# Performance work log

Measured on AMD Instinct MI355X. Metric: run time of the kernel, lower is better.

Reference implementation:

```python
import jax, jax.numpy as jnp
import numpy as np

# Per-layer (in_dim, hidden) for the 6 stacked LSTM layers:
# rnn_inp: (1,64),(64,64),(64,64); rnn_out: (64,1),(1,1),(1,1)
_LAYER_DIMS = [(1, 64), (64, 64), (64, 64), (64, 1), (1, 1), (1, 1)]
_LAYER_NAMES = ['a0', 'a1', 'a2', 'b0', 'b1', 'b2']


def _lstm_layer(x, w_ih, w_hh, b_ih, b_hh):
    """Single unidirectional LSTM layer, PyTorch gate order (i, f, g, o).
    x: [B, T, Din]; w_ih: [4H, Din]; w_hh: [4H, H]; biases: [4H]. Returns [B, T, H]."""
    H = w_hh.shape[1]
    B = x.shape[0]
    # Input projection for all timesteps at once (one big GEMM).
    pre = jnp.einsum('btd,gd->btg', x, w_ih) + b_ih + b_hh  # [B, T, 4H]
    pre_t = jnp.swapaxes(pre, 0, 1)  # [T, B, 4H]

    def step(carry, xt):
        h, c = carry
        gates = xt + h @ w_hh.T  # [B, 4H]
        i, f, g, o = jnp.split(gates, 4, axis=-1)
        i = jax.nn.sigmoid(i)
        f = jax.nn.sigmoid(f)
        g = jnp.tanh(g)
        o = jax.nn.sigmoid(o)
        c = f * c + i * g
        h = o * jnp.tanh(c)
        return (h, c), h

    h0 = jnp.zeros((B, H), x.dtype)
    (_, _), hs = jax.lax.scan(step, (h0, h0), pre_t)  # hs: [T, B, H]
    return jnp.swapaxes(hs, 0, 1)


def setup_inputs() -> dict:
    key = jax.random.key(0)
    B, T = 256, 512
    inp = {}
    k, key = jax.random.split(key)
    inp['x'] = jax.random.normal(k, (B, T, 1), dtype=jnp.float32)
    for name, (din, h) in zip(_LAYER_NAMES, _LAYER_DIMS):
        s = 1.0 / np.sqrt(h)  # PyTorch LSTM init scale U(-1/sqrt(H), 1/sqrt(H))
        k1, k2, k3, k4, key = jax.random.split(key, 5)
        inp[f'w_ih_{name}'] = jax.random.uniform(k1, (4 * h, din), jnp.float32, -s, s)
        inp[f'w_hh_{name}'] = jax.random.uniform(k2, (4 * h, h), jnp.float32, -s, s)
        inp[f'b_ih_{name}'] = jax.random.uniform(k3, (4 * h,), jnp.float32, -s, s)
        inp[f'b_hh_{name}'] = jax.random.uniform(k4, (4 * h,), jnp.float32, -s, s)
    return inp


def reference(x,
              w_ih_a0, w_hh_a0, b_ih_a0, b_hh_a0,
              w_ih_a1, w_hh_a1, b_ih_a1, b_hh_a1,
              w_ih_a2, w_hh_a2, b_ih_a2, b_hh_a2,
              w_ih_b0, w_hh_b0, b_ih_b0, b_hh_b0,
              w_ih_b1, w_hh_b1, b_ih_b1, b_hh_b1,
              w_ih_b2, w_hh_b2, b_ih_b2, b_hh_b2):
    layers = [
        (w_ih_a0, w_hh_a0, b_ih_a0, b_hh_a0),
        (w_ih_a1, w_hh_a1, b_ih_a1, b_hh_a1),
        (w_ih_a2, w_hh_a2, b_ih_a2, b_hh_a2),
        (w_ih_b0, w_hh_b0, b_ih_b0, b_hh_b0),
        (w_ih_b1, w_hh_b1, b_ih_b1, b_hh_b1),
        (w_ih_b2, w_hh_b2, b_ih_b2, b_hh_b2),
    ]
    h = x
    for w_ih, w_hh, b_ih, b_hh in layers:
        h = _lstm_layer(h, w_ih, w_hh, b_ih, b_hh)
    # activation between the two LSTM stacks is identity (activation_type='identity')
    return h  # [B, T, 1]
```

## Files before the change

### kernel.cpp

```cpp
#include <hip/hip_runtime.h>


#define BB 256
#define TT 512
#define CH 8
#define NS 16
#define NW (TT / CH)
#define HP 72
#define PP 260

typedef _Float16 v2h __attribute__((ext_vector_type(2)));
typedef _Float16 v8h __attribute__((ext_vector_type(8)));
typedef float v4f __attribute__((ext_vector_type(4)));

__device__ __forceinline__ float sig_(float x) {
  return __builtin_amdgcn_rcpf(1.f + __builtin_amdgcn_exp2f(-1.44269504f * x));
}
__device__ __forceinline__ float tanh_(float x) {
  return __builtin_fmaf(2.f, __builtin_amdgcn_rcpf(1.f + __builtin_amdgcn_exp2f(-2.88539008f * x)), -1.f);
}

template <int K>
__device__ __forceinline__ float qb_(float v) {
  return __int_as_float(__builtin_amdgcn_update_dpp(
      0, __float_as_int(v), (K | (K << 2) | (K << 4) | (K << 6)), 0xF, 0xF, true));
}

#if __has_builtin(__builtin_amdgcn_fdot2)
#define FDOT2(acc, a, b) (acc) = __builtin_amdgcn_fdot2((a), (b), (acc), false)
#else
#define FDOT2(acc, a, b) \
  (acc) = __builtin_fmaf((float)(a)[0], (float)(b)[0], \
          __builtin_fmaf((float)(a)[1], (float)(b)[1], (acc)))
#endif
#define KEEPP(a) asm volatile("" : "+v"(a))
#define PIN32(w)                                                            \
  do {                                                                      \
    _Pragma("unroll") for (int _i = 0; _i < 32; ++_i) KEEPP((w)[_i]);       \
  } while (0)
#define PIN16(w)                                                            \
  do {                                                                      \
    _Pragma("unroll") for (int _i = 0; _i < 16; ++_i) KEEPP((w)[_i]);       \
  } while (0)

#define WAITP(i, v)                                                           \
  while (__hip_atomic_load(&prog[i], __ATOMIC_ACQUIRE,                        \
                           __HIP_MEMORY_SCOPE_WORKGROUP) < (v)) {             \
    __builtin_amdgcn_s_sleep(1);                                              \
  }
#define POSTP(i, v)                                                           \
  do {                                                                        \
    asm volatile("s_waitcnt lgkmcnt(0)" ::: "memory");                        \
    if (lane == 0)                                                            \
      __hip_atomic_store(&prog[i], (v), __ATOMIC_RELEASE,                     \
                         __HIP_MEMORY_SCOPE_WORKGROUP);                       \
  } while (0)

__device__ __forceinline__ v2h bc2h_(int v) { return __builtin_bit_cast(v2h, v); }

__device__ __forceinline__ void load_h64(const _Float16* p, v2h hv[32]) {
  const int4* hp = reinterpret_cast<const int4*>(p);
#pragma unroll
  for (int i = 0; i < 8; ++i) {
    int4 blk = hp[i];
    hv[4 * i + 0] = bc2h_(blk.x);
    hv[4 * i + 1] = bc2h_(blk.y);
    hv[4 * i + 2] = bc2h_(blk.z);
    hv[4 * i + 3] = bc2h_(blk.w);
  }
}

__device__ __forceinline__ void load_row16(const float* src, v2h dst[32]) {
  const float4* p = reinterpret_cast<const float4*>(src);
#pragma unroll
  for (int i = 0; i < 16; ++i) {
    float4 v = p[i];
    dst[2 * i]     = v2h{(_Float16)v.x, (_Float16)v.y};
    dst[2 * i + 1] = v2h{(_Float16)v.z, (_Float16)v.w};
  }
}

__device__ __forceinline__ void load_row_pair(const float* src, v2h* lo, v2h* hi) {
  const float4* p = reinterpret_cast<const float4*>(src);
#pragma unroll
  for (int i = 0; i < 8; ++i) {
    float4 v = p[i];
    lo[2 * i]     = v2h{(_Float16)v.x, (_Float16)v.y};
    lo[2 * i + 1] = v2h{(_Float16)v.z, (_Float16)v.w};
  }
#pragma unroll
  for (int i = 0; i < 8; ++i) {
    float4 v = p[8 + i];
    hi[2 * i]     = v2h{(_Float16)v.x, (_Float16)v.y};
    hi[2 * i + 1] = v2h{(_Float16)v.z, (_Float16)v.w};
  }
}

__device__ __forceinline__ v8h ldbfrag_(const float* W, int t, int kc, int lane) {
  const int row = 16 * t + (lane & 15);
  const float* p = W + row * 64 + 32 * kc + 4 * (lane >> 4);
  float4 fa = *reinterpret_cast<const float4*>(p);
  float4 fb = *reinterpret_cast<const float4*>(p + 16);
  return v8h{(_Float16)fa.x, (_Float16)fa.y, (_Float16)fa.z, (_Float16)fa.w,
             (_Float16)fb.x, (_Float16)fb.y, (_Float16)fb.z, (_Float16)fb.w};
}

__device__ __forceinline__ void dot4_(const v2h w[4][32], const v2h hv[32],
                                      float& p0, float& p1, float& p2, float& p3) {
  float a0 = p0, a1 = p1, a2 = p2, a3 = p3;
  float b0 = 0.f, b1 = 0.f, b2 = 0.f, b3 = 0.f;
#pragma unroll
  for (int j = 0; j < 32; j += 2) {
    FDOT2(a0, w[0][j], hv[j]);         FDOT2(a1, w[1][j], hv[j]);
    FDOT2(a2, w[2][j], hv[j]);         FDOT2(a3, w[3][j], hv[j]);
    FDOT2(b0, w[0][j + 1], hv[j + 1]); FDOT2(b1, w[1][j + 1], hv[j + 1]);
    FDOT2(b2, w[2][j + 1], hv[j + 1]); FDOT2(b3, w[3][j + 1], hv[j + 1]);
  }
  p0 = a0 + b0; p1 = a1 + b1; p2 = a2 + b2; p3 = a3 + b3;
}

__global__ __attribute__((amdgpu_flat_work_group_size(384, 384),
                          amdgpu_waves_per_eu(2, 2)))
void lstm_pipe_k(
    const float* __restrict__ x,
    const float* __restrict__ wih_a0, const float* __restrict__ whh_a0,
    const float* __restrict__ bih_a0, const float* __restrict__ bhh_a0,
    const float* __restrict__ wih_a1, const float* __restrict__ whh_a1,
    const float* __restrict__ bih_a1, const float* __restrict__ bhh_a1,
    const float* __restrict__ wih_a2, const float* __restrict__ whh_a2,
    const float* __restrict__ bih_a2, const float* __restrict__ bhh_a2,
    const float* __restrict__ wih_b0, const float* __restrict__ whh_b0,
    const float* __restrict__ bih_b0, const float* __restrict__ bhh_b0,
    const float* __restrict__ wih_b1, const float* __restrict__ whh_b1,
    const float* __restrict__ bih_b1, const float* __restrict__ bhh_b1,
    const float* __restrict__ wih_b2, const float* __restrict__ whh_b2,
    const float* __restrict__ bih_b2, const float* __restrict__ bhh_b2,
    float* __restrict__ out)
{
  const int b = blockIdx.x;
  const int tid = threadIdx.x;
  const int wave = tid >> 6;
  const int lane = tid & 63;

  __shared__ __align__(16) _Float16 hh[3][NS][HP];
  __shared__ __align__(16) float pj[2][NS][PP];
  __shared__ float xs[TT];
  __shared__ int prog[6];

  for (int i = tid; i < TT; i += 384) xs[i] = x[(size_t)b * TT + i];
  for (int i = tid; i < 3 * NS * HP / 2; i += 384) reinterpret_cast<int*>(hh)[i] = 0;
  if (tid < 6) prog[tid] = 0;

  union UW {
    v2h wt[4][32];
    v8h bfr[16][2];
  } u;

  float bias[4] = {0.f, 0.f, 0.f, 0.f};
  float wi0_[4] = {0.f, 0.f, 0.f, 0.f};
  float whb0[4] = {}, wi1b[4] = {}, wh1b[4] = {}, bb1[4] = {},
        wi2b[4] = {}, wh2b[4] = {}, bb2[4] = {};

  if (wave == 0) {
#pragma unroll
    for (int q = 0; q < 4; ++q) {
      const int row = q * 64 + lane;
      load_row16(whh_a0 + row * 64, u.wt[q]);
      bias[q] = bih_a0[row] + bhh_a0[row];
      wi0_[q] = wih_a0[row];
    }
    PIN32(u.wt[0]); PIN32(u.wt[1]); PIN32(u.wt[2]); PIN32(u.wt[3]);
  } else if (wave == 1) {
#pragma unroll
    for (int q = 0; q < 4; ++q) {
      const int row = q * 64 + lane;
      load_row16(whh_a1 + row * 64, u.wt[q]);
      bias[q] = bih_a1[row] + bhh_a1[row];
    }
    PIN32(u.wt[0]); PIN32(u.wt[1]); PIN32(u.wt[2]); PIN32(u.wt[3]);
  } else if (wave == 2) {
#pragma unroll
    for (int q = 0; q < 4; ++q) {
      const int row = q * 64 + lane;
      load_row16(whh_a2 + row * 64, u.wt[q]);
      bias[q] = bih_a2[row] + bhh_a2[row];
    }
    PIN32(u.wt[0]); PIN32(u.wt[1]); PIN32(u.wt[2]); PIN32(u.wt[3]);
  } else if (wave == 3) {
    const int q = lane & 3;
    load_row_pair(wih_b0 + q * 64, u.wt[0], u.wt[1]);
    bias[0] = bih_b0[q] + bhh_b0[q];
#pragma unroll
    for (int k = 0; k < 4; ++k) {
      whb0[k] = whh_b0[k];
      wi1b[k] = wih_b1[k]; wh1b[k] = whh_b1[k]; bb1[k] = bih_b1[k] + bhh_b1[k];
      wi2b[k] = wih_b2[k]; wh2b[k] = whh_b2[k]; bb2[k] = bih_b2[k] + bhh_b2[k];
    }
    PIN16(u.wt[0]); PIN16(u.wt[1]);
  } else if (wave == 4) {
#pragma unroll
    for (int t = 0; t < 16; ++t) {
      u.bfr[t][0] = ldbfrag_(wih_a1, t, 0, lane);
      u.bfr[t][1] = ldbfrag_(wih_a1, t, 1, lane);
    }
  } else {
#pragma unroll
    for (int t = 0; t < 16; ++t) {
      u.bfr[t][0] = ldbfrag_(wih_a2, t, 0, lane);
      u.bfr[t][1] = ldbfrag_(wih_a2, t, 1, lane);
    }
  }
  __syncthreads();

  float c = 0.f;
  float h0b = 0.f, c0b = 0.f, h1b = 0.f, c1b = 0.f, h2b = 0.f, c2b = 0.f;

  if (wave == 0) {
    __builtin_amdgcn_s_setprio(1);
    for (int k = 0; k < NW; ++k) {
      if (k >= 2) { WAITP(4, k - 1); }
      const int t0 = k * CH;
      for (int s = 0; s < CH; ++s) {
        const int t = t0 + s;
        v2h hv[32];
        load_h64(&hh[0][(t + NS - 1) & (NS - 1)][0], hv);
        const float xv = xs[t];
        float p0 = bias[0], p1 = bias[1], p2 = bias[2], p3 = bias[3];
        dot4_(u.wt, hv, p0, p1, p2, p3);
        p0 = __builtin_fmaf(wi0_[0], xv, p0);
        p1 = __builtin_fmaf(wi0_[1], xv, p1);
        p2 = __builtin_fmaf(wi0_[2], xv, p2);
        p3 = __builtin_fmaf(wi0_[3], xv, p3);
        float gi = sig_(p0), gf = sig_(p1), gg = tanh_(p2), go = sig_(p3);
        c = __builtin_fmaf(gf, c, gi * gg);
        hh[0][t & (NS - 1)][lane] = (_Float16)(go * tanh_(c));
      }
      POSTP(0, k + 1);
    }
    __builtin_amdgcn_s_setprio(0);
  } else if (wave == 1) {
    __builtin_amdgcn_s_setprio(1);
    for (int k = 0; k < NW; ++k) {
      WAITP(4, k + 1);
      if (k >= 2) { WAITP(5, k - 1); }
      const int t0 = k * CH;
      for (int s = 0; s < CH; ++s) {
        const int t = t0 + s;
        v2h hv[32];
        load_h64(&hh[1][(t + NS - 1) & (NS - 1)][0], hv);
        float4 pr = *reinterpret_cast<const float4*>(&pj[0][t & (NS - 1)][lane * 4]);
        float p0 = bias[0], p1 = bias[1], p2 = bias[2], p3 = bias[3];
        dot4_(u.wt, hv, p0, p1, p2, p3);
        p0 += pr.x; p1 += pr.y; p2 += pr.z; p3 += pr.w;
        float gi = sig_(p0), gf = sig_(p1), gg = tanh_(p2), go = sig_(p3);
        c = __builtin_fmaf(gf, c, gi * gg);
        hh[1][t & (NS - 1)][lane] = (_Float16)(go * tanh_(c));
      }
      POSTP(1, k + 1);
    }
    __builtin_amdgcn_s_setprio(0);
  } else if (wave == 2) {
    __builtin_amdgcn_s_setprio(1);
    for (int k = 0; k < NW; ++k) {
      WAITP(5, k + 1);
      if (k >= 2) { WAITP(3, k - 1); }
      const int t0 = k * CH;
      for (int s = 0; s < CH; ++s) {
        const int t = t0 + s;
        v2h hv[32];
        load_h64(&hh[2][(t + NS - 1) & (NS - 1)][0], hv);
        float4 pr = *reinterpret_cast<const float4*>(&pj[1][t & (NS - 1)][lane * 4]);
        float p0 = bias[0], p1 = bias[1], p2 = bias[2], p3 = bias[3];
        dot4_(u.wt, hv, p0, p1, p2, p3);
        p0 += pr.x; p1 += pr.y; p2 += pr.z; p3 += pr.w;
        float gi = sig_(p0), gf = sig_(p1), gg = tanh_(p2), go = sig_(p3);
        c = __builtin_fmaf(gf, c, gi * gg);
        hh[2][t & (NS - 1)][lane] = (_Float16)(go * tanh_(c));
      }
      POSTP(2, k + 1);
    }
    __builtin_amdgcn_s_setprio(0);
  } else if (wave == 3) {
    for (int k = 0; k < NW; ++k) {
      WAITP(2, k + 1);
      const int t0 = k * CH;
      for (int s = 0; s < CH; ++s) {
        const int t = t0 + s;
        v2h hv[32];
        load_h64(&hh[2][t & (NS - 1)][0], hv);
        float pga = bias[0], pgb = 0.f;
#pragma unroll
        for (int j = 0; j < 16; ++j) {
          FDOT2(pga, u.wt[0][j], hv[j]);
          FDOT2(pgb, u.wt[1][j], hv[16 + j]);
        }
        float pg = pga + pgb;
        float p_i = qb_<0>(pg), p_f = qb_<1>(pg), p_g = qb_<2>(pg), p_o = qb_<3>(pg);
        float i0 = sig_(__builtin_fmaf(whb0[0], h0b, p_i));
        float f0 = sig_(__builtin_fmaf(whb0[1], h0b, p_f));
        float g0 = tanh_(__builtin_fmaf(whb0[2], h0b, p_g));
        float o0 = sig_(__builtin_fmaf(whb0[3], h0b, p_o));
        c0b = __builtin_fmaf(f0, c0b, i0 * g0);
        h0b = o0 * tanh_(c0b);
        float i1 = sig_(bb1[0] + __builtin_fmaf(wi1b[0], h0b, wh1b[0] * h1b));
        float f1 = sig_(bb1[1] + __builtin_fmaf(wi1b[1], h0b, wh1b[1] * h1b));
        float g1 = tanh_(bb1[2] + __builtin_fmaf(wi1b[2], h0b, wh1b[2] * h1b));
        float o1 = sig_(bb1[3] + __builtin_fmaf(wi1b[3], h0b, wh1b[3] * h1b));
        c1b = __builtin_fmaf(f1, c1b, i1 * g1);
        h1b = o1 * tanh_(c1b);
        float i2 = sig_(bb2[0] + __builtin_fmaf(wi2b[0], h1b, wh2b[0] * h2b));
        float f2 = sig_(bb2[1] + __builtin_fmaf(wi2b[1], h1b, wh2b[1] * h2b));
        float g2 = tanh_(bb2[2] + __builtin_fmaf(wi2b[2], h1b, wh2b[2] * h2b));
        float o2 = sig_(bb2[3] + __builtin_fmaf(wi2b[3], h1b, wh2b[3] * h2b));
        c2b = __builtin_fmaf(f2, c2b, i2 * g2);
        h2b = o2 * tanh_(c2b);
        if (lane == 0) out[(size_t)b * TT + t] = h2b;
      }
      POSTP(3, k + 1);
    }
  } else if (wave == 4) {
    for (int k = 0; k < NW; ++k) {
      WAITP(0, k + 1);
      if (k >= 2) { WAITP(1, k - 1); }
      const int t0 = k * CH;
      const int slotb = (t0 + (lane & 15)) & (NS - 1);
      const char* hp = (const char*)(&hh[0][slotb][0]) + 8 * (lane >> 4);
      int2 r00 = *(const int2*)(hp);
      int2 r01 = *(const int2*)(hp + 32);
      int2 r10 = *(const int2*)(hp + 64);
      int2 r11 = *(const int2*)(hp + 96);
      v8h Bf0 = __builtin_bit_cast(v8h, int4{r00.x, r00.y, r01.x, r01.y});
      v8h Bf1 = __builtin_bit_cast(v8h, int4{r10.x, r10.y, r11.x, r11.y});
      float* pbase = &pj[0][slotb][0] + 16 * (lane >> 4);
      const bool wr = (lane & 15) < 8;
      const v4f z = {0.f, 0.f, 0.f, 0.f};
#pragma unroll
      for (int tl = 0; tl < 16; ++tl) {
        v4f acc = __builtin_amdgcn_mfma_f32_16x16x32_f16(u.bfr[tl][0], Bf0, z, 0, 0, 0);
        acc = __builtin_amdgcn_mfma_f32_16x16x32_f16(u.bfr[tl][1], Bf1, acc, 0, 0, 0);
        if (wr) {
          const int o = 64 * (tl & 3) + (tl >> 2);
          pbase[o] = acc[0]; pbase[o + 4] = acc[1];
          pbase[o + 8] = acc[2]; pbase[o + 12] = acc[3];
        }
        __builtin_amdgcn_sched_barrier(0);
      }
      POSTP(4, k + 1);
    }
  } else {
    for (int k = 0; k < NW; ++k) {
      WAITP(1, k + 1);
      if (k >= 2) { WAITP(2, k - 1); }
      const int t0 = k * CH;
      const int slotb = (t0 + (lane & 15)) & (NS - 1);
      const char* hp = (const char*)(&hh[1][slotb][0]) + 8 * (lane >> 4);
      int2 r00 = *(const int2*)(hp);
      int2 r01 = *(const int2*)(hp + 32);
      int2 r10 = *(const int2*)(hp + 64);
      int2 r11 = *(const int2*)(hp + 96);
      v8h Bf0 = __builtin_bit_cast(v8h, int4{r00.x, r00.y, r01.x, r01.y});
      v8h Bf1 = __builtin_bit_cast(v8h, int4{r10.x, r10.y, r11.x, r11.y});
      float* pbase = &pj[1][slotb][0] + 16 * (lane >> 4);
      const bool wr = (lane & 15) < 8;
      const v4f z = {0.f, 0.f, 0.f, 0.f};
#pragma unroll
      for (int tl = 0; tl < 16; ++tl) {
        v4f acc = __builtin_amdgcn_mfma_f32_16x16x32_f16(u.bfr[tl][0], Bf0, z, 0, 0, 0);
        acc = __builtin_amdgcn_mfma_f32_16x16x32_f16(u.bfr[tl][1], Bf1, acc, 0, 0, 0);
        if (wr) {
          const int o = 64 * (tl & 3) + (tl >> 2);
          pbase[o] = acc[0]; pbase[o + 4] = acc[1];
          pbase[o + 8] = acc[2]; pbase[o + 12] = acc[3];
        }
        __builtin_amdgcn_sched_barrier(0);
      }
      POSTP(5, k + 1);
    }
  }
}

extern "C" void kernel_launch(void* const* d_in, const int* in_sizes, int n_in,
                              void* d_out, int out_size, void* d_ws, size_t ws_size,
                              hipStream_t stream) {
  const float* x      = (const float*)d_in[0];
  const float* wih_a0 = (const float*)d_in[1];
  const float* whh_a0 = (const float*)d_in[2];
  const float* bih_a0 = (const float*)d_in[3];
  const float* bhh_a0 = (const float*)d_in[4];
  const float* wih_a1 = (const float*)d_in[5];
  const float* whh_a1 = (const float*)d_in[6];
  const float* bih_a1 = (const float*)d_in[7];
  const float* bhh_a1 = (const float*)d_in[8];
  const float* wih_a2 = (const float*)d_in[9];
  const float* whh_a2 = (const float*)d_in[10];
  const float* bih_a2 = (const float*)d_in[11];
  const float* bhh_a2 = (const float*)d_in[12];
  const float* wih_b0 = (const float*)d_in[13];
  const float* whh_b0 = (const float*)d_in[14];
  const float* bih_b0 = (const float*)d_in[15];
  const float* bhh_b0 = (const float*)d_in[16];
  const float* wih_b1 = (const float*)d_in[17];
  const float* whh_b1 = (const float*)d_in[18];
  const float* bih_b1 = (const float*)d_in[19];
  const float* bhh_b1 = (const float*)d_in[20];
  const float* wih_b2 = (const float*)d_in[21];
  const float* whh_b2 = (const float*)d_in[22];
  const float* bih_b2 = (const float*)d_in[23];
  const float* bhh_b2 = (const float*)d_in[24];
  float* out = (float*)d_out;

  lstm_pipe_k<<<BB, 384, 0, stream>>>(
      x,
      wih_a0, whh_a0, bih_a0, bhh_a0,
      wih_a1, whh_a1, bih_a1, bhh_a1,
      wih_a2, whh_a2, bih_a2, bhh_a2,
      wih_b0, whh_b0, bih_b0, bhh_b0,
      wih_b1, whh_b1, bih_b1, bhh_b1,
      wih_b2, whh_b2, bih_b2, bhh_b2,
      out);
}
```

Before: 347.5 us.

## Use MFMA for recurrent h@W_hh in 64-wide LSTM waves and shrink chunk size

Replaces the per-lane fdot2 dot products for the recurrent matrix-vector product in the three 64-hidden layers with MFMA 16x16x32 f16 ops. The weight fragments are loaded in MFMA B layout and the needed output column is picked out per lane with selects. The pipeline chunk size drops from 8 to 4 timesteps and the dependency waits are adjusted, which shortens pipeline fill latency between stages. This wastes most of each MFMA, since only one row of the 16-row A tile is used, and it adds selection overhead per step.

Result: faster. 338.4 us (-2.6%).

```diff
diff --git a/kernel.cpp b/kernel.cpp
--- a/kernel.cpp
+++ b/kernel.cpp
@@ -3,7 +3,7 @@
 
 #define BB 256
 #define TT 512
-#define CH 8
+#define CH 4
 #define NS 16
 #define NW (TT / CH)
 #define HP 72
@@ -34,10 +34,6 @@
           __builtin_fmaf((float)(a)[1], (float)(b)[1], (acc)))
 #endif
 #define KEEPP(a) asm volatile("" : "+v"(a))
-#define PIN32(w)                                                            \
-  do {                                                                      \
-    _Pragma("unroll") for (int _i = 0; _i < 32; ++_i) KEEPP((w)[_i]);       \
-  } while (0)
 #define PIN16(w)                                                            \
   do {                                                                      \
     _Pragma("unroll") for (int _i = 0; _i < 16; ++_i) KEEPP((w)[_i]);       \
@@ -70,16 +66,6 @@
   }
 }
 
-__device__ __forceinline__ void load_row16(const float* src, v2h dst[32]) {
-  const float4* p = reinterpret_cast<const float4*>(src);
-#pragma unroll
-  for (int i = 0; i < 16; ++i) {
-    float4 v = p[i];
-    dst[2 * i]     = v2h{(_Float16)v.x, (_Float16)v.y};
-    dst[2 * i + 1] = v2h{(_Float16)v.z, (_Float16)v.w};
-  }
-}
-
 __device__ __forceinline__ void load_row_pair(const float* src, v2h* lo, v2h* hi) {
   const float4* p = reinterpret_cast<const float4*>(src);
 #pragma unroll
@@ -103,20 +89,6 @@
   float4 fb = *reinterpret_cast<const float4*>(p + 16);
   return v8h{(_Float16)fa.x, (_Float16)fa.y, (_Float16)fa.z, (_Float16)fa.w,
              (_Float16)fb.x, (_Float16)fb.y, (_Float16)fb.z, (_Float16)fb.w};
-}
-
-__device__ __forceinline__ void dot4_(const v2h w[4][32], const v2h hv[32],
-                                      float& p0, float& p1, float& p2, float& p3) {
-  float a0 = p0, a1 = p1, a2 = p2, a3 = p3;
-  float b0 = 0.f, b1 = 0.f, b2 = 0.f, b3 = 0.f;
-#pragma unroll
-  for (int j = 0; j < 32; j += 2) {
-    FDOT2(a0, w[0][j], hv[j]);         FDOT2(a1, w[1][j], hv[j]);
-    FDOT2(a2, w[2][j], hv[j]);         FDOT2(a3, w[3][j], hv[j]);
-    FDOT2(b0, w[0][j + 1], hv[j + 1]); FDOT2(b1, w[1][j + 1], hv[j + 1]);
-    FDOT2(b2, w[2][j + 1], hv[j + 1]); FDOT2(b3, w[3][j + 1], hv[j + 1]);
-  }
-  p0 = a0 + b0; p1 = a1 + b1; p2 = a2 + b2; p3 = a3 + b3;
 }
 
 __global__ __attribute__((amdgpu_flat_work_group_size(384, 384),
@@ -152,8 +124,8 @@
   if (tid < 6) prog[tid] = 0;
 
   union UW {
-    v2h wt[4][32];
     v8h bfr[16][2];
+    v2h wtb[2][16];
   } u;
 
   float bias[4] = {0.f, 0.f, 0.f, 0.f};
@@ -163,32 +135,35 @@
 
   if (wave == 0) {
 #pragma unroll
+    for (int t = 0; t < 16; ++t) {
+      u.bfr[t][0] = ldbfrag_(whh_a0, t, 0, lane);
+      u.bfr[t][1] = ldbfrag_(whh_a0, t, 1, lane);
+    }
+#pragma unroll
     for (int q = 0; q < 4; ++q) {
       const int row = q * 64 + lane;
-      load_row16(whh_a0 + row * 64, u.wt[q]);
       bias[q] = bih_a0[row] + bhh_a0[row];
       wi0_[q] = wih_a0[row];
     }
-    PIN32(u.wt[0]); PIN32(u.wt[1]); PIN32(u.wt[2]); PIN32(u.wt[3]);
   } else if (wave == 1) {
 #pragma unroll
-    for (int q = 0; q < 4; ++q) {
-      const int row = q * 64 + lane;
-      load_row16(whh_a1 + row * 64, u.wt[q]);
-      bias[q] = bih_a1[row] + bhh_a1[row];
-    }
-    PIN32(u.wt[0]); PIN32(u.wt[1]); PIN32(u.wt[2]); PIN32(u.wt[3]);
+    for (int t = 0; t < 16; ++t) {
+      u.bfr[t][0] = ldbfrag_(whh_a1, t, 0, lane);
+      u.bfr[t][1] = ldbfrag_(whh_a1, t, 1, lane);
+    }
+#pragma unroll
+    for (int q = 0; q < 4; ++q) bias[q] = bih_a1[q * 64 + lane] + bhh_a1[q * 64 + lane];
   } else if (wave == 2) {
 #pragma unroll
-    for (int q = 0; q < 4; ++q) {
-      const int row = q * 64 + lane;
-      load_row16(whh_a2 + row * 64, u.wt[q]);
-      bias[q] = bih_a2[row] + bhh_a2[row];
-    }
-    PIN32(u.wt[0]); PIN32(u.wt[1]); PIN32(u.wt[2]); PIN32(u.wt[3]);
+    for (int t = 0; t < 16; ++t) {
+      u.bfr[t][0] = ldbfrag_(whh_a2, t, 0, lane);
+      u.bfr[t][1] = ldbfrag_(whh_a2, t, 1, lane);
+    }
+#pragma unroll
+    for (int q = 0; q < 4; ++q) bias[q] = bih_a2[q * 64 + lane] + bhh_a2[q * 64 + lane];
   } else if (wave == 3) {
     const int q = lane & 3;
-    load_row_pair(wih_b0 + q * 64, u.wt[0], u.wt[1]);
+    load_row_pair(wih_b0 + q * 64, u.wtb[0], u.wtb[1]);
     bias[0] = bih_b0[q] + bhh_b0[q];
 #pragma unroll
     for (int k = 0; k < 4; ++k) {
@@ -196,7 +171,7 @@
       wi1b[k] = wih_b1[k]; wh1b[k] = whh_b1[k]; bb1[k] = bih_b1[k] + bhh_b1[k];
       wi2b[k] = wih_b2[k]; wh2b[k] = whh_b2[k]; bb2[k] = bih_b2[k] + bhh_b2[k];
     }
-    PIN16(u.wt[0]); PIN16(u.wt[1]);
+    PIN16(u.wtb[0]); PIN16(u.wtb[1]);
   } else if (wave == 4) {
 #pragma unroll
     for (int t = 0; t < 16; ++t) {
@@ -214,23 +189,42 @@
 
   float c = 0.f;
   float h0b = 0.f, c0b = 0.f, h1b = 0.f, c1b = 0.f, h2b = 0.f, c2b = 0.f;
+  const int q4 = lane >> 4;
+  const bool s0 = q4 & 1, s1 = q4 & 2;
+  const v4f z = {0.f, 0.f, 0.f, 0.f};
 
   if (wave == 0) {
     __builtin_amdgcn_s_setprio(1);
     for (int k = 0; k < NW; ++k) {
-      if (k >= 2) { WAITP(4, k - 1); }
+      if (k >= 4) { WAITP(4, k - 3); }
       const int t0 = k * CH;
       for (int s = 0; s < CH; ++s) {
         const int t = t0 + s;
-        v2h hv[32];
-        load_h64(&hh[0][(t + NS - 1) & (NS - 1)][0], hv);
+        const char* hp = (const char*)(&hh[0][(t + NS - 1) & (NS - 1)][0]) + 8 * q4;
+        int2 r00 = *(const int2*)(hp);
+        int2 r01 = *(const int2*)(hp + 32);
+        int2 r10 = *(const int2*)(hp + 64);
+        int2 r11 = *(const int2*)(hp + 96);
+        v8h A0 = __builtin_bit_cast(v8h, int4{r00.x, r00.y, r01.x, r01.y});
+        v8h A1 = __builtin_bit_cast(v8h, int4{r10.x, r10.y, r11.x, r11.y});
+        v4f acc[16];
+#pragma unroll
+        for (int tl = 0; tl < 16; ++tl) {
+          v4f d = __builtin_amdgcn_mfma_f32_16x16x32_f16(A0, u.bfr[tl][0], z, 0, 0, 0);
+          acc[tl] = __builtin_amdgcn_mfma_f32_16x16x32_f16(A1, u.bfr[tl][1], d, 0, 0, 0);
+        }
+        float p[4];
+#pragma unroll
+        for (int g = 0; g < 4; ++g) {
+          float v01 = s0 ? acc[4 * g + 1][0] : acc[4 * g + 0][0];
+          float v23 = s0 ? acc[4 * g + 3][0] : acc[4 * g + 2][0];
+          p[g] = s1 ? v23 : v01;
+        }
         const float xv = xs[t];
-        float p0 = bias[0], p1 = bias[1], p2 = bias[2], p3 = bias[3];
-        dot4_(u.wt, hv, p0, p1, p2, p3);
-        p0 = __builtin_fmaf(wi0_[0], xv, p0);
-        p1 = __builtin_fmaf(wi0_[1], xv, p1);
-        p2 = __builtin_fmaf(wi0_[2], xv, p2);
-        p3 = __builtin_fmaf(wi0_[3], xv, p3);
+        float p0 = __builtin_fmaf(wi0_[0], xv, p[0] + bias[0]);
+        float p1 = __builtin_fmaf(wi0_[1], xv, p[1] + bias[1]);
+        float p2 = __builtin_fmaf(wi0_[2], xv, p[2] + bias[2]);
+        float p3 = __builtin_fmaf(wi0_[3], xv, p[3] + bias[3]);
         float gi = sig_(p0), gf = sig_(p1), gg = tanh_(p2), go = sig_(p3);
         c = __builtin_fmaf(gf, c, gi * gg);
         hh[0][t & (NS - 1)][lane] = (_Float16)(go * tanh_(c));
@@ -242,16 +236,35 @@
     __builtin_amdgcn_s_setprio(1);
     for (int k = 0; k < NW; ++k) {
       WAITP(4, k + 1);
-      if (k >= 2) { WAITP(5, k - 1); }
+      if (k >= 4) { WAITP(5, k - 3); }
       const int t0 = k * CH;
       for (int s = 0; s < CH; ++s) {
         const int t = t0 + s;
-        v2h hv[32];
-        load_h64(&hh[1][(t + NS - 1) & (NS - 1)][0], hv);
+        const char* hp = (const char*)(&hh[1][(t + NS - 1) & (NS - 1)][0]) + 8 * q4;
+        int2 r00 = *(const int2*)(hp);
+        int2 r01 = *(const int2*)(hp + 32);
+        int2 r10 = *(const int2*)(hp + 64);
+        int2 r11 = *(const int2*)(hp + 96);
+        v8h A0 = __builtin_bit_cast(v8h, int4{r00.x, r00.y, r01.x, r01.y});
+        v8h A1 = __builtin_bit_cast(v8h, int4{r10.x, r10.y, r11.x, r11.y});
         float4 pr = *reinterpret_cast<const float4*>(&pj[0][t & (NS - 1)][lane * 4]);
-        float p0 = bias[0], p1 = bias[1], p2 = bias[2], p3 = bias[3];
-        dot4_(u.wt, hv, p0, p1, p2, p3);
-        p0 += pr.x; p1 += pr.y; p2 += pr.z; p3 += pr.w;
+        v4f acc[16];
+#pragma unroll
+        for (int tl = 0; tl < 16; ++tl) {
+          v4f d = __builtin_amdgcn_mfma_f32_16x16x32_f16(A0, u.bfr[tl][0], z, 0, 0, 0);
+          acc[tl] = __builtin_amdgcn_mfma_f32_16x16x32_f16(A1, u.bfr[tl][1], d, 0, 0, 0);
+        }
+        float p[4];
+#pragma unroll
+        for (int g = 0; g < 4; ++g) {
+          float v01 = s0 ? acc[4 * g + 1][0] : acc[4 * g + 0][0];
+          float v23 = s0 ? acc[4 * g + 3][0] : acc[4 * g + 2][0];
+          p[g] = s1 ? v23 : v01;
+        }
+        float p0 = p[0] + bias[0] + pr.x;
+        float p1 = p[1] + bias[1] + pr.y;
+        float p2 = p[2] + bias[2] + pr.z;
+        float p3 = p[3] + bias[3] + pr.w;
         float gi = sig_(p0), gf = sig_(p1), gg = tanh_(p2), go = sig_(p3);
         c = __builtin_fmaf(gf, c, gi * gg);
         hh[1][t & (NS - 1)][lane] = (_Float16)(go * tanh_(c));
@@ -263,16 +276,35 @@
     __builtin_amdgcn_s_setprio(1);
     for (int k = 0; k < NW; ++k) {
       WAITP(5, k + 1);
-      if (k >= 2) { WAITP(3, k - 1); }
+      if (k >= 4) { WAITP(3, k - 3); }
       const int t0 = k * CH;
       for (int s = 0; s < CH; ++s) {
         const int t = t0 + s;
-        v2h hv[32];
-        load_h64(&hh[2][(t + NS - 1) & (NS - 1)][0], hv);
+        const char* hp = (const char*)(&hh[2][(t + NS - 1) & (NS - 1)][0]) + 8 * q4;
+        int2 r00 = *(const int2*)(hp);
+        int2 r01 = *(const int2*)(hp + 32);
+        int2 r10 = *(const int2*)(hp + 64);
+        int2 r11 = *(const int2*)(hp + 96);
+        v8h A0 = __builtin_bit_cast(v8h, int4{r00.x, r00.y, r01.x, r01.y});
+        v8h A1 = __builtin_bit_cast(v8h, int4{r10.x, r10.y, r11.x, r11.y});
         float4 pr = *reinterpret_cast<const float4*>(&pj[1][t & (NS - 1)][lane * 4]);
-        float p0 = bias[0], p1 = bias[1], p2 = bias[2], p3 = bias[3];
-        dot4_(u.wt, hv, p0, p1, p2, p3);
-        p0 += pr.x; p1 += pr.y; p2 += pr.z; p3 += pr.w;
+        v4f acc[16];
+#pragma unroll
+        for (int tl = 0; tl < 16; ++tl) {
+          v4f d = __builtin_amdgcn_mfma_f32_16x16x32_f16(A0, u.bfr[tl][0], z, 0, 0, 0);
+          acc[tl] = __builtin_amdgcn_mfma_f32_16x16x32_f16(A1, u.bfr[tl][1], d, 0, 0, 0);
+        }
+        float p[4];
+#pragma unroll
+        for (int g = 0; g < 4; ++g) {
+          float v01 = s0 ? acc[4 * g + 1][0] : acc[4 * g + 0][0];
+          float v23 = s0 ? acc[4 * g + 3][0] : acc[4 * g + 2][0];
+          p[g] = s1 ? v23 : v01;
+        }
+        float p0 = p[0] + bias[0] + pr.x;
+        float p1 = p[1] + bias[1] + pr.y;
+        float p2 = p[2] + bias[2] + pr.z;
+        float p3 = p[3] + bias[3] + pr.w;
         float gi = sig_(p0), gf = sig_(p1), gg = tanh_(p2), go = sig_(p3);
         c = __builtin_fmaf(gf, c, gi * gg);
         hh[2][t & (NS - 1)][lane] = (_Float16)(go * tanh_(c));
@@ -291,8 +323,8 @@
         float pga = bias[0], pgb = 0.f;
 #pragma unroll
         for (int j = 0; j < 16; ++j) {
-          FDOT2(pga, u.wt[0][j], hv[j]);
-          FDOT2(pgb, u.wt[1][j], hv[16 + j]);
+          FDOT2(pga, u.wtb[0][j], hv[j]);
+          FDOT2(pgb, u.wtb[1][j], hv[16 + j]);
         }
         float pg = pga + pgb;
         float p_i = qb_<0>(pg), p_f = qb_<1>(pg), p_g = qb_<2>(pg), p_o = qb_<3>(pg);
@@ -321,19 +353,18 @@
   } else if (wave == 4) {
     for (int k = 0; k < NW; ++k) {
       WAITP(0, k + 1);
-      if (k >= 2) { WAITP(1, k - 1); }
+      if (k >= 4) { WAITP(1, k - 3); }
       const int t0 = k * CH;
       const int slotb = (t0 + (lane & 15)) & (NS - 1);
-      const char* hp = (const char*)(&hh[0][slotb][0]) + 8 * (lane >> 4);
+      const char* hp = (const char*)(&hh[0][slotb][0]) + 8 * q4;
       int2 r00 = *(const int2*)(hp);
       int2 r01 = *(const int2*)(hp + 32);
       int2 r10 = *(const int2*)(hp + 64);
       int2 r11 = *(const int2*)(hp + 96);
       v8h Bf0 = __builtin_bit_cast(v8h, int4{r00.x, r00.y, r01.x, r01.y});
       v8h Bf1 = __builtin_bit_cast(v8h, int4{r10.x, r10.y, r11.x, r11.y});
-      float* pbase = &pj[0][slotb][0] + 16 * (lane >> 4);
-      const bool wr = (lane & 15) < 8;
-      const v4f z = {0.f, 0.f, 0.f, 0.f};
+      float* pbase = &pj[0][slotb][0] + 16 * q4;
+      const bool wr = (lane & 15) < CH;
 #pragma unroll
       for (int tl = 0; tl < 16; ++tl) {
         v4f acc = __builtin_amdgcn_mfma_f32_16x16x32_f16(u.bfr[tl][0], Bf0, z, 0, 0, 0);
@@ -350,19 +381,18 @@
   } else {
     for (int k = 0; k < NW; ++k) {
       WAITP(1, k + 1);
-      if (k >= 2) { WAITP(2, k - 1); }
+      if (k >= 4) { WAITP(2, k - 3); }
       const int t0 = k * CH;
       const int slotb = (t0 + (lane & 15)) & (NS - 1);
-      const char* hp = (const char*)(&hh[1][slotb][0]) + 8 * (lane >> 4);
+      const char* hp = (const char*)(&hh[1][slotb][0]) + 8 * q4;
       int2 r00 = *(const int2*)(hp);
       int2 r01 = *(const int2*)(hp + 32);
       int2 r10 = *(const int2*)(hp + 64);
       int2 r11 = *(const int2*)(hp + 96);
       v8h Bf0 = __builtin_bit_cast(v8h, int4{r00.x, r00.y, r01.x, r01.y});
       v8h Bf1 = __builtin_bit_cast(v8h, int4{r10.x, r10.y, r11.x, r11.y});
-      float* pbase = &pj[1][slotb][0] + 16 * (lane >> 4);
-      const bool wr = (lane & 15) < 8;
-      const v4f z = {0.f, 0.f, 0.f, 0.f};
+      float* pbase = &pj[1][slotb][0] + 16 * q4;
+      const bool wr = (lane & 15) < CH;
 #pragma unroll
       for (int tl = 0; tl < 16; ++tl) {
         v4f acc = __builtin_amdgcn_mfma_f32_16x16x32_f16(u.bfr[tl][0], Bf0, z, 0, 0, 0);
```
